# Optimization experiments

Hardware: AMD Instinct MI355X
Metric: run time of the kernel (lower is better)

Reference implementation:

```python
import jax, jax.numpy as jnp
import numpy as np

B, T, DIM, H = 2, 2048, 1024, 16
HD = DIM // H


def setup_inputs() -> dict:
    key = jax.random.key(0)
    k1, k2, k3 = jax.random.split(key, 3)
    std = 1.0 / np.sqrt(DIM)
    x = jax.random.normal(k1, (B, T, DIM), dtype=jnp.float32)
    # torch Linear(dim, 3*dim).weight is [3*dim, dim]; we store the transposed
    # [dim, 3*dim] layout so forward is x @ W_qkv (same math).
    W_qkv = jax.random.uniform(k2, (DIM, 3 * DIM), dtype=jnp.float32, minval=-std, maxval=std)
    W_proj = jax.random.uniform(k3, (DIM, DIM), dtype=jnp.float32, minval=-std, maxval=std)
    return {"x": x, "W_qkv": W_qkv, "W_proj": W_proj}


def reference(x, W_qkv, W_proj):
    Bv, Tv, C = x.shape
    # qkv projection -> [B, T, 3, H, HD] -> q,k,v each [B, H, T, HD]
    qkv = (x @ W_qkv).reshape(Bv, Tv, 3, H, HD)
    qkv = jnp.transpose(qkv, (2, 0, 3, 1, 4))
    q, k, v = qkv[0], qkv[1], qkv[2]
    scale = jnp.asarray(np.sqrt(HD), dtype=x.dtype)
    scores = jnp.einsum('bhqd,bhkd->bhqk', q, k) / scale
    causal = jnp.tril(jnp.ones((Tv, Tv), dtype=bool))  # [T, T]
    scores = jnp.where(causal[None, None, :, :], scores, -jnp.inf)
    attn = jax.nn.softmax(scores, axis=-1)  # [B, H, T, T]
    # entropy per query position, averaged over heads -> [B, T]
    entropy = -(attn * jnp.log(attn + 1e-9)).sum(axis=-1).mean(axis=1)
    # dropout is identity in eval mode
    out = jnp.einsum('bhqk,bhkd->bhqd', attn, v)
    out = jnp.transpose(out, (0, 2, 1, 3)).reshape(Bv, Tv, C)
    return out @ W_proj, entropy
```

## Files before the change

kernel.cpp:

```cpp
#include <hip/hip_runtime.h>


typedef unsigned short u16;
typedef __attribute__((ext_vector_type(8))) __bf16 bf16x8;
typedef __attribute__((ext_vector_type(4))) float float4v;

#define BQ 2
#define TQ 2048
#define DIMQ 1024
#define HQ 16
#define HDQ 64

__device__ __forceinline__ float4v mfma16(bf16x8 a, bf16x8 b, float4v c) {
    return __builtin_amdgcn_mfma_f32_16x16x32_bf16(a, b, c, 0, 0, 0);
}

__device__ __forceinline__ u16 f2bf(float f) {
    unsigned x = __float_as_uint(f);
    return (u16)((x + 0x7FFFu + ((x >> 16) & 1u)) >> 16);
}

__device__ __forceinline__ uint4 cvt8(float4 a, float4 b) {
    union { uint4 v; u16 u[8]; } r;
    r.u[0] = f2bf(a.x); r.u[1] = f2bf(a.y); r.u[2] = f2bf(a.z); r.u[3] = f2bf(a.w);
    r.u[4] = f2bf(b.x); r.u[5] = f2bf(b.y); r.u[6] = f2bf(b.z); r.u[7] = f2bf(b.w);
    return r.v;
}

__device__ __forceinline__ void async16(const u16* g, u16* l) {
    __builtin_amdgcn_global_load_lds(
        (const __attribute__((address_space(1))) void*)g,
        (__attribute__((address_space(3))) void*)l, 16, 0, 0);
}

__device__ __forceinline__ void tr_tile(
    const float* __restrict__ in, u16* __restrict__ out, int R, int C,
    int tx, int ty, int tid, float (*T)[68])
{
    const int k0 = ty * 64, n0 = tx * 64;
    {
        int r = tid >> 2, cc = (tid & 3) << 4;
        const float* src = in + (size_t)(k0 + r) * C + n0 + cc;
        float4 v0 = ((const float4*)src)[0];
        float4 v1 = ((const float4*)src)[1];
        float4 v2 = ((const float4*)src)[2];
        float4 v3 = ((const float4*)src)[3];
        *(float4*)&T[r][cc + 0]  = v0;
        *(float4*)&T[r][cc + 4]  = v1;
        *(float4*)&T[r][cc + 8]  = v2;
        *(float4*)&T[r][cc + 12] = v3;
    }
    __syncthreads();
    {
        int nr = tid >> 2, kc = (tid & 3) << 4;
        union { uint4 v; u16 u[8]; } o0, o1;
#pragma unroll
        for (int j = 0; j < 8; ++j) o0.u[j] = f2bf(T[kc + j][nr]);
#pragma unroll
        for (int j = 0; j < 8; ++j) o1.u[j] = f2bf(T[kc + 8 + j][nr]);
        u16* dst = out + (size_t)(n0 + nr) * R + k0 + kc;
        ((uint4*)dst)[0] = o0.v;
        *(uint4*)(dst + 8) = o1.v;
    }
}

__global__ __launch_bounds__(256) void prep_kernel(
    const float* __restrict__ x, const float* __restrict__ Wq,
    const float* __restrict__ Wp,
    u16* __restrict__ xb, u16* __restrict__ Wt, u16* __restrict__ Wpt)
{
    __shared__ float T[64][68];
    const int bx = blockIdx.x, tid = threadIdx.x;
    if (bx < 2048) {
        int i = (bx * 256 + tid) * 8;
        float4 a = *(const float4*)(x + i);
        float4 b = *(const float4*)(x + i + 4);
        *(uint4*)(xb + i) = cvt8(a, b);
    } else if (bx < 2816) {
        int bb = bx - 2048;
        tr_tile(Wq, Wt, DIMQ, 3 * DIMQ, bb % 48, bb / 48, tid, T);
    } else {
        int bb = bx - 2816;
        tr_tile(Wp, Wpt, DIMQ, DIMQ, bb & 15, bb >> 4, tid, T);
    }
}

__global__ __launch_bounds__(256) void tr_cvt(
    const float* __restrict__ in, u16* __restrict__ out, int R, int C)
{
    __shared__ float T[64][68];
    tr_tile(in, out, R, C, blockIdx.x, blockIdx.y, threadIdx.x, T);
}

template <int TILEM, int MODE>
__global__ __launch_bounds__(256) void gemm_db(
    const u16* __restrict__ A, const u16* __restrict__ Bt,
    int M, int N, int K,
    u16* __restrict__ Qo, u16* __restrict__ Ko, u16* __restrict__ Vt,
    float* __restrict__ Of, const float* __restrict__ EntIn)
{
    constexpr int MT = TILEM / 32;
    constexpr int AR = TILEM / 64;
    __shared__ u16 As[2][TILEM * 32];
    __shared__ u16 Bs[2][128 * 32];

    const int tid = threadIdx.x;
    const int bm = blockIdx.y, bn = blockIdx.x;
    const int wave = tid >> 6, lane = tid & 63;
    const int quad = lane >> 4, c = lane & 15;
    const int wm = wave >> 1, wn = wave & 1;
    const int x3 = c & 3;

    const float4v z = {0.f, 0.f, 0.f, 0.f};
    float4v acc[MT][4];
#pragma unroll
    for (int mt = 0; mt < MT; ++mt)
#pragma unroll
        for (int tn = 0; tn < 4; ++tn) acc[mt][tn] = z;

    const int srow = tid >> 2;
    const int schunk8 = (((tid & 3) ^ (srow & 3)) << 3);
    const u16* ga = A  + (size_t)(bm * TILEM + srow) * K + schunk8;
    const u16* gb = Bt + (size_t)(bn * 128  + srow) * K + schunk8;

#pragma unroll
    for (int p = 0; p < AR; ++p)
        async16(ga + (size_t)(p * 64) * K, As[0] + p * 2048 + tid * 8);
#pragma unroll
    for (int p = 0; p < 2; ++p)
        async16(gb + (size_t)(p * 64) * K, Bs[0] + p * 2048 + tid * 8);

    const int niter = K >> 5;
    for (int it = 0; it < niter; ++it) {
        __syncthreads();
        if (it + 1 < niter) {
            const int nb = (it + 1) & 1;
            const int kc = (it + 1) * 32;
#pragma unroll
            for (int p = 0; p < AR; ++p)
                async16(ga + kc + (size_t)(p * 64) * K, As[nb] + p * 2048 + tid * 8);
#pragma unroll
            for (int p = 0; p < 2; ++p)
                async16(gb + kc + (size_t)(p * 64) * K, Bs[nb] + p * 2048 + tid * 8);
        }
        const u16* as = As[it & 1];
        const u16* bs = Bs[it & 1];

        bf16x8 af[MT], bfr[4];
#pragma unroll
        for (int mt = 0; mt < MT; ++mt)
            af[mt] = *(const bf16x8*)&as[(wm * (TILEM / 2) + mt * 16 + c) * 32 +
                                         ((quad ^ x3) << 3)];
#pragma unroll
        for (int tn = 0; tn < 4; ++tn)
            bfr[tn] = *(const bf16x8*)&bs[(wn * 64 + tn * 16 + c) * 32 +
                                          ((quad ^ x3) << 3)];
#pragma unroll
        for (int mt = 0; mt < MT; ++mt)
#pragma unroll
            for (int tn = 0; tn < 4; ++tn)
                acc[mt][tn] = mfma16(af[mt], bfr[tn], acc[mt][tn]);
    }

#pragma unroll
    for (int mt = 0; mt < MT; ++mt)
#pragma unroll
        for (int tn = 0; tn < 4; ++tn) {
            int gm0 = bm * TILEM + wm * (TILEM / 2) + mt * 16 + quad * 4;
            int gn  = bn * 128 + wn * 64 + tn * 16 + c;
            if (MODE == 0) {
                int s = gn >> 10, h = (gn >> 6) & 15, d = gn & 63;
                int b = gm0 >> 11, t0 = gm0 & 2047;
                size_t bh = (size_t)(b * HQ + h);
                if (s == 2) {
                    union { unsigned long long w; u16 u[4]; } pk;
#pragma unroll
                    for (int r = 0; r < 4; ++r) pk.u[r] = f2bf(acc[mt][tn][r]);
                    *(unsigned long long*)&Vt[(bh * HDQ + d) * TQ + t0] = pk.w;
                } else {
                    u16* dst = (s == 0) ? Qo : Ko;
                    float sc = (s == 0) ? 0.18033688f : 1.0f;
#pragma unroll
                    for (int r = 0; r < 4; ++r)
                        dst[(bh * TQ + t0 + r) * HDQ + d] = f2bf(acc[mt][tn][r] * sc);
                }
            } else {
#pragma unroll
                for (int r = 0; r < 4; ++r)
                    Of[(size_t)(gm0 + r) * N + gn] = acc[mt][tn][r];
            }
        }

    if (MODE == 1 && bn == 0 && bm < 16) {
        int i = bm * 256 + tid;
        int b = i >> 11, t = i & 2047;
        float s = 0.f;
#pragma unroll
        for (int h = 0; h < HQ; ++h) s += EntIn[((size_t)(b * HQ + h)) * TQ + t];
        Of[(size_t)BQ * TQ * DIMQ + i] = s * (1.0f / HQ);
    }
}

__global__ __launch_bounds__(256) void attn_kernel(
    const u16* __restrict__ Q, const u16* __restrict__ K,
    const u16* __restrict__ Vt, u16* __restrict__ AO,
    float* __restrict__ Ent)
{
    const int d = blockIdx.x;
    const int bh = (d & 7) * 4 + ((d >> 3) >> 4);
    const int pt = (d >> 3) & 15;
    const int qt1 = pt;
    const int qt2 = 31 - pt;

    const int tid = threadIdx.x;
    const int wave = tid >> 6, lane = tid & 63;
    const int quad = lane >> 4, c = lane & 15;
    const int x7 = c & 7;

    __shared__ u16 Ks[2][64 * 64];
    __shared__ u16 Vs[2][64 * 64];
    __shared__ u16 Ps[4][16 * 64];

    const u16* Qp = Q  + (size_t)bh * TQ * HDQ;
    const u16* Kp = K  + (size_t)bh * TQ * HDQ;
    const u16* Vp = Vt + (size_t)bh * HDQ * TQ;

    const int q0[2] = { qt1 * 64 + wave * 16, qt2 * 64 + wave * 16 };

    bf16x8 qf[2][2];
#pragma unroll
    for (int s = 0; s < 2; ++s) {
        const u16* qr = Qp + (size_t)(q0[s] + c) * HDQ;
        qf[s][0] = *(const bf16x8*)(qr + quad * 8);
        qf[s][1] = *(const bf16x8*)(qr + 32 + quad * 8);
    }

    const float MX2 = 17.312336f;
    const float4v z = {0.f, 0.f, 0.f, 0.f};
    const float4v mz = {-MX2, -MX2, -MX2, -MX2};
    float4v oacc[2][4];
#pragma unroll
    for (int s = 0; s < 2; ++s)
#pragma unroll
        for (int tn = 0; tn < 4; ++tn) oacc[s][tn] = z;
    float lp[2] = {0.f, 0.f}, tp[2] = {0.f, 0.f};

    u16* psw = &Ps[wave][0];
    const int ntile = qt2 + 1;

    const int srow = tid >> 3;
    const int schunk8 = (((tid & 7) ^ (srow & 7)) << 3);
    const u16* ka = Kp + (size_t)srow * HDQ + schunk8;
    const u16* va = Vp + (size_t)srow * TQ + schunk8;

    {
        async16(ka, Ks[0] + tid * 8);
        async16(ka + (size_t)32 * HDQ, Ks[0] + 2048 + tid * 8);
        async16(va, Vs[0] + tid * 8);
        async16(va + (size_t)32 * TQ, Vs[0] + 2048 + tid * 8);
    }

    for (int jt = 0; jt < ntile; ++jt) {
        __syncthreads();
        if (jt + 1 < ntile) {
            int nb = (jt + 1) & 1;
            async16(ka + (size_t)((jt + 1) * 64) * HDQ, Ks[nb] + tid * 8);
            async16(ka + (size_t)((jt + 1) * 64 + 32) * HDQ, Ks[nb] + 2048 + tid * 8);
            async16(va + (jt + 1) * 64, Vs[nb] + tid * 8);
            async16(va + (size_t)32 * TQ + (jt + 1) * 64, Vs[nb] + 2048 + tid * 8);
        }
        const u16* ksb = Ks[jt & 1];
        const u16* vsb = Vs[jt & 1];

        bf16x8 kf[4][2], vf[4][2];
#pragma unroll
        for (int tn = 0; tn < 4; ++tn) {
            int base = (tn * 16 + c) * 64;
            kf[tn][0] = *(const bf16x8*)&ksb[base + ((quad ^ x7) << 3)];
            kf[tn][1] = *(const bf16x8*)&ksb[base + (((quad + 4) ^ x7) << 3)];
            vf[tn][0] = *(const bf16x8*)&vsb[base + ((quad ^ x7) << 3)];
            vf[tn][1] = *(const bf16x8*)&vsb[base + (((quad + 4) ^ x7) << 3)];
        }

#pragma unroll
        for (int s = 0; s < 2; ++s) {
            if (s == 0 && jt > qt1) continue;
            const int diag = s ? qt2 : qt1;
#pragma unroll
            for (int tn = 0; tn < 4; ++tn) {
                float4v sacc = mz;
                sacc = mfma16(kf[tn][0], qf[s][0], sacc);
                sacc = mfma16(kf[tn][1], qf[s][1], sacc);
                if (jt == diag) {
#pragma unroll
                    for (int r = 0; r < 4; ++r) {
                        int kg = jt * 64 + tn * 16 + quad * 4 + r;
                        if (kg > q0[s] + c) sacc[r] = -1e30f;
                    }
                }
                float pv[4];
#pragma unroll
                for (int r = 0; r < 4; ++r) {
                    float sv = sacc[r];
                    float p;
                    asm("v_exp_f32 %0, %1" : "=v"(p) : "v"(sv));
                    lp[s] += p;
                    tp[s] += p * sv;
                    pv[r] = p;
                }
                uint2 pk;
                asm("v_cvt_pk_bf16_f32 %0, %1, %2"
                    : "=v"(pk.x) : "v"(pv[0]), "v"(pv[1]));
                asm("v_cvt_pk_bf16_f32 %0, %1, %2"
                    : "=v"(pk.y) : "v"(pv[2]), "v"(pv[3]));
                int kc8 = tn * 2 + (quad >> 1);
                *(uint2*)&psw[c * 64 + ((kc8 ^ x7) << 3) + (quad & 1) * 4] = pk;
            }
            bf16x8 pf0 = *(const bf16x8*)&psw[c * 64 + ((quad ^ x7) << 3)];
            bf16x8 pf1 = *(const bf16x8*)&psw[c * 64 + (((quad + 4) ^ x7) << 3)];
            __builtin_amdgcn_s_setprio(1);
#pragma unroll
            for (int tn = 0; tn < 4; ++tn) {
                oacc[s][tn] = mfma16(vf[tn][0], pf0, oacc[s][tn]);
                oacc[s][tn] = mfma16(vf[tn][1], pf1, oacc[s][tn]);
            }
            __builtin_amdgcn_s_setprio(0);
        }
    }

#pragma unroll
    for (int s = 0; s < 2; ++s) {
        lp[s] += __shfl_xor(lp[s], 16); lp[s] += __shfl_xor(lp[s], 32);
        tp[s] += __shfl_xor(tp[s], 16); tp[s] += __shfl_xor(tp[s], 32);
    }

    const int b = bh >> 4, h = bh & 15;
#pragma unroll
    for (int s = 0; s < 2; ++s) {
        float inv = 1.0f / lp[s];
        u16* dst = AO + ((size_t)(b * TQ + q0[s] + c)) * DIMQ + h * HDQ;
#pragma unroll
        for (int tn = 0; tn < 4; ++tn) {
            unsigned u[4];
#pragma unroll
            for (int r = 0; r < 4; ++r)
                u[r] = (unsigned)f2bf(oacc[s][tn][r] * inv);
            uint2 pk;
            pk.x = u[0] | (u[1] << 16);
            pk.y = u[2] | (u[3] << 16);
            *(uint2*)(dst + tn * 16 + quad * 4) = pk;
        }
        if (quad == 0)
            Ent[(size_t)bh * TQ + q0[s] + c] =
                logf(lp[s]) - 0.69314718f * tp[s] / lp[s];
    }
}

extern "C" void kernel_launch(void* const* d_in, const int* in_sizes, int n_in,
                              void* d_out, int out_size, void* d_ws, size_t ws_size,
                              hipStream_t stream) {
    const float* x     = (const float*)d_in[0];
    const float* Wqkv  = (const float*)d_in[1];
    const float* Wproj = (const float*)d_in[2];
    float* out = (float*)d_out;

    const size_t NE = (size_t)BQ * HQ * TQ * HDQ;
    const size_t WQN = (size_t)3 * DIMQ * DIMQ;
    const size_t WPN = (size_t)DIMQ * DIMQ;
    u16* Qb  = (u16*)d_ws;
    u16* Kb  = Qb + NE;
    u16* Vtb = Kb + NE;
    u16* xb  = Vtb + NE;
    u16* Wt  = xb + NE;
    u16* AO  = xb;

    const size_t need = (4 * NE + WQN + WPN) * 2 + (size_t)BQ * HQ * TQ * 4;
    const bool room = ws_size >= need;
    u16* Wpt = room ? (Wt + WQN) : Wt;
    float* Ent = room ? (float*)(Wpt + WPN) : (float*)(Wt + WQN);

    prep_kernel<<<dim3(room ? 3072 : 2816), 256, 0, stream>>>(
        x, Wqkv, Wproj, xb, Wt, Wpt);
    gemm_db<128, 0><<<dim3(24, 32), 256, 0, stream>>>(
        xb, Wt, BQ * TQ, 3 * DIMQ, DIMQ, Qb, Kb, Vtb, nullptr, nullptr);
    if (!room)
        tr_cvt<<<dim3(16, 16), 256, 0, stream>>>(Wproj, Wpt, DIMQ, DIMQ);
    attn_kernel<<<dim3(512), 256, 0, stream>>>(Qb, Kb, Vtb, AO, Ent);
    gemm_db<64, 1><<<dim3(8, 64), 256, 0, stream>>>(
        AO, Wpt, BQ * TQ, DIMQ, DIMQ, nullptr, nullptr, nullptr, out, Ent);
}
```

Before: 176.2 us.

## Replace LDS round-trip for P with permlane swaps; rebalance attention tile order

The attention kernel now rearranges the bf16 softmax probabilities into MFMA B-operand layout in registers, using v_permlane32/16 swaps instead of writing them to a per-wave LDS buffer and reading them back. This removes LDS stores and loads plus their latency from the inner loop and frees shared memory. The block-to-query-tile mapping is also reversed for half the blocks to change the order of the paired causal work. The output projection GEMM switches to 128-row tiles with half as many blocks, which gives more reuse per block but less parallelism. The lane-swap mapping must exactly match the previous LDS layout, otherwise results are wrong.

```diff
diff --git a/kernel.cpp b/kernel.cpp
--- a/kernel.cpp
+++ b/kernel.cpp
@@ -31,6 +31,11 @@
     __builtin_amdgcn_global_load_lds(
         (const __attribute__((address_space(1))) void*)g,
         (__attribute__((address_space(3))) void*)l, 16, 0, 0);
+}
+
+__device__ __forceinline__ void plswap(unsigned& a, unsigned& b) {
+    asm("v_permlane32_swap_b32 %0, %1" : "+v"(a), "+v"(b));
+    asm("v_permlane16_swap_b32 %0, %1" : "+v"(a), "+v"(b));
 }
 
 __device__ __forceinline__ void tr_tile(
@@ -148,7 +153,7 @@
 
         bf16x8 af[MT], bfr[4];
 #pragma unroll
-        for (int mt = 0; mt < MT; ++mt)
+    for (int mt = 0; mt < MT; ++mt)
             af[mt] = *(const bf16x8*)&as[(wm * (TILEM / 2) + mt * 16 + c) * 32 +
                                          ((quad ^ x3) << 3)];
 #pragma unroll
@@ -207,8 +212,10 @@
     float* __restrict__ Ent)
 {
     const int d = blockIdx.x;
-    const int bh = (d & 7) * 4 + ((d >> 3) >> 4);
-    const int pt = (d >> 3) & 15;
+    const int j = d >> 3;
+    const int bh = (d & 7) * 4 + (j >> 4);
+    int pt = j & 15;
+    if (j & 32) pt = 15 - pt;
     const int qt1 = pt;
     const int qt2 = 31 - pt;
 
@@ -219,7 +226,6 @@
 
     __shared__ u16 Ks[2][64 * 64];
     __shared__ u16 Vs[2][64 * 64];
-    __shared__ u16 Ps[4][16 * 64];
 
     const u16* Qp = Q  + (size_t)bh * TQ * HDQ;
     const u16* Kp = K  + (size_t)bh * TQ * HDQ;
@@ -245,7 +251,6 @@
         for (int tn = 0; tn < 4; ++tn) oacc[s][tn] = z;
     float lp[2] = {0.f, 0.f}, tp[2] = {0.f, 0.f};
 
-    u16* psw = &Ps[wave][0];
     const int ntile = qt2 + 1;
 
     const int srow = tid >> 3;
@@ -286,6 +291,7 @@
         for (int s = 0; s < 2; ++s) {
             if (s == 0 && jt > qt1) continue;
             const int diag = s ? qt2 : qt1;
+            unsigned w0[4], w1[4];
 #pragma unroll
             for (int tn = 0; tn < 4; ++tn) {
                 float4v sacc = mz;
@@ -308,21 +314,23 @@
                     tp[s] += p * sv;
                     pv[r] = p;
                 }
-                uint2 pk;
                 asm("v_cvt_pk_bf16_f32 %0, %1, %2"
-                    : "=v"(pk.x) : "v"(pv[0]), "v"(pv[1]));
+                    : "=v"(w0[tn]) : "v"(pv[0]), "v"(pv[1]));
                 asm("v_cvt_pk_bf16_f32 %0, %1, %2"
-                    : "=v"(pk.y) : "v"(pv[2]), "v"(pv[3]));
-                int kc8 = tn * 2 + (quad >> 1);
-                *(uint2*)&psw[c * 64 + ((kc8 ^ x7) << 3) + (quad & 1) * 4] = pk;
+                    : "=v"(w1[tn]) : "v"(pv[2]), "v"(pv[3]));
             }
-            bf16x8 pf0 = *(const bf16x8*)&psw[c * 64 + ((quad ^ x7) << 3)];
-            bf16x8 pf1 = *(const bf16x8*)&psw[c * 64 + (((quad + 4) ^ x7) << 3)];
+            plswap(w0[0], w0[1]);
+            plswap(w1[0], w1[1]);
+            plswap(w0[2], w0[3]);
+            plswap(w1[2], w1[3]);
+            union { uint4 u; bf16x8 v; } P0, P1;
+            P0.u = (uint4){w0[0], w1[0], w0[1], w1[1]};
+            P1.u = (uint4){w0[2], w1[2], w0[3], w1[3]};
             __builtin_amdgcn_s_setprio(1);
 #pragma unroll
             for (int tn = 0; tn < 4; ++tn) {
-                oacc[s][tn] = mfma16(vf[tn][0], pf0, oacc[s][tn]);
-                oacc[s][tn] = mfma16(vf[tn][1], pf1, oacc[s][tn]);
+                oacc[s][tn] = mfma16(vf[tn][0], P0.v, oacc[s][tn]);
+                oacc[s][tn] = mfma16(vf[tn][1], P1.v, oacc[s][tn]);
             }
             __builtin_amdgcn_s_setprio(0);
         }
@@ -386,6 +394,6 @@
     if (!room)
         tr_cvt<<<dim3(16, 16), 256, 0, stream>>>(Wproj, Wpt, DIMQ, DIMQ);
     attn_kernel<<<dim3(512), 256, 0, stream>>>(Qb, Kb, Vtb, AO, Ent);
-    gemm_db<64, 1><<<dim3(8, 64), 256, 0, stream>>>(
+    gemm_db<128, 1><<<dim3(8, 32), 256, 0, stream>>>(
         AO, Wpt, BQ * TQ, DIMQ, DIMQ, nullptr, nullptr, nullptr, out, Ent);
 }
```

After: 179.2 us. No clear change (+1.7%).
